# Performance work log

Measured on AMD Instinct MI355X. Metric: run time of the kernel, lower is better.

Reference implementation:

```python
import jax, jax.numpy as jnp
import numpy as np

NUM_NODES = 100000   # KG entity count (embedding table)
N_SUB = 20000        # subgraph nodes
E = 400000           # edges
R = 16               # num_rels
B = 8                # num_bases (block-diagonal decomposition)
H = 256              # h_dim (submat = H // B = 32)
PAIRS = 4096         # DTI drug-target pairs


def _rgcn_bdd_layer(x, src, dst, etype, norm, W, loop_w, bias):
    """DGL RelGraphConv with 'bdd' regularizer, self_loop=True, activation=None.

    message_e = blockdiag(W[etype_e]) @ x[src_e] * norm_e ; out_v = sum_e->v message_e
    By linearity we first segment-sum norm-scaled source features per (dst, rel)
    bucket, then apply the R relation block transforms once per node -- same math,
    no per-edge weight gather.
    """
    N, h = x.shape
    si = h // B  # block input size == block output size here
    contrib = x[src] * norm                      # [E, H]
    seg = dst * R + etype                        # bucket per (dst node, relation)
    agg = jax.ops.segment_sum(contrib, seg, num_segments=N * R)
    agg = agg.reshape(N, R, B, si)               # [N, R, B, si]
    msg = jnp.einsum('nrbi,rbio->nbo', agg, W).reshape(N, h)
    return msg + bias + x @ loop_w               # self-loop + bias (activation=None)


def setup_inputs() -> dict:
    key = jax.random.key(0)
    ks = jax.random.split(key, 20)
    si = H // B
    inp = {
        'drugs_index': jax.random.randint(ks[0], (PAIRS,), 0, N_SUB, dtype=jnp.int32),
        'targets_index': jax.random.randint(ks[1], (PAIRS,), 0, N_SUB, dtype=jnp.int32),
        'node_ids': jax.random.randint(ks[2], (N_SUB,), 0, NUM_NODES, dtype=jnp.int32),
        'src': jax.random.randint(ks[3], (E,), 0, N_SUB, dtype=jnp.int32),
        'dst': jax.random.randint(ks[4], (E,), 0, N_SUB, dtype=jnp.int32),
        'etype': jax.random.randint(ks[5], (E,), 0, R, dtype=jnp.int32),
        'norm': jax.random.uniform(ks[6], (E, 1), dtype=jnp.float32),
    }
    s_h = 1.0 / np.sqrt(H)
    s_blk = 1.0 / np.sqrt(si)
    inp['emb'] = jax.random.normal(ks[7], (NUM_NODES, H), jnp.float32)
    inp['w1'] = jax.random.normal(ks[8], (R, B, si, si), jnp.float32) * s_blk
    inp['loop_w1'] = jax.random.normal(ks[9], (H, H), jnp.float32) * s_h
    inp['b1'] = jnp.zeros((H,), jnp.float32)
    inp['w2'] = jax.random.normal(ks[10], (R, B, si, si), jnp.float32) * s_blk
    inp['loop_w2'] = jax.random.normal(ks[11], (H, H), jnp.float32) * s_h
    inp['b2'] = jnp.zeros((H,), jnp.float32)
    d = 2 * H
    inp['fc1_W'] = jax.random.normal(ks[12], (d, d), jnp.float32) / np.sqrt(d)
    inp['fc1_b'] = jnp.zeros((d,), jnp.float32)
    inp['fc2_W'] = jax.random.normal(ks[13], (d, 1), jnp.float32) / np.sqrt(d)
    inp['fc2_b'] = jnp.zeros((1,), jnp.float32)
    return inp


def reference(drugs_index, targets_index, node_ids, src, dst, etype, norm,
              emb, w1, loop_w1, b1, w2, loop_w2, b2,
              fc1_W, fc1_b, fc2_W, fc2_b):
    h = emb[node_ids]                                      # EmbeddingLayer
    h = _rgcn_bdd_layer(h, src, dst, etype, norm, w1, loop_w1, b1)
    h = _rgcn_bdd_layer(h, src, dst, etype, norm, w2, loop_w2, b2)
    x = jnp.concatenate([h[drugs_index], h[targets_index]], axis=1)  # [PAIRS, 2H]
    x = jax.nn.relu(x @ fc1_W + fc1_b)                     # dropout=0 -> identity
    return jax.nn.sigmoid(x @ fc2_W + fc2_b)               # [PAIRS, 1]
```

## Files before the change

### kernel.cpp

```cpp
#include <hip/hip_runtime.h>
#include <math.h>

typedef __attribute__((ext_vector_type(8))) short short8;
typedef __attribute__((ext_vector_type(4))) float f32x4;
typedef __attribute__((ext_vector_type(4))) _Float16 half4;
typedef __attribute__((ext_vector_type(8))) _Float16 half8;

#define N_SUBN   20000
#define E_EDGES  400000
#define R_REL    16
#define H_DIM    256
#define NBINS    (N_SUBN * R_REL)
#define SCAN_CHUNK 2048
#define NSCAN_BLOCKS ((NBINS + SCAN_CHUNK - 1) / SCAN_CHUNK)
#define NPAIRS   4096
#define TILE_N   32
#define NT_BLOCKS (N_SUBN / TILE_N)
#define D2       512
#define ECAP     1024

__device__ __forceinline__ ushort f2bf(float x) {
    uint u = __float_as_uint(x);
    u += 0x7fffu + ((u >> 16) & 1u);
    return (ushort)(u >> 16);
}
__device__ __forceinline__ float bf2f(ushort h) {
    return __uint_as_float(((uint)h) << 16);
}

__global__ void k_count(const int* __restrict__ dst, const int* __restrict__ ety,
                        int* __restrict__ cnt) {
    int e = blockIdx.x * 256 + threadIdx.x;
    if (e < E_EDGES) atomicAdd(&cnt[dst[e] * R_REL + ety[e]], 1);
}

__global__ void k_scan1(int* __restrict__ data, int* __restrict__ bs) {
    __shared__ int ts[256];
    int base = blockIdx.x * SCAN_CHUNK + threadIdx.x * 8;
    int v[8]; int s = 0;
#pragma unroll
    for (int j = 0; j < 8; j++) {
        int idx = base + j;
        v[j] = (idx < NBINS) ? data[idx] : 0;
        s += v[j];
    }
    ts[threadIdx.x] = s;
    __syncthreads();
    for (int off = 1; off < 256; off <<= 1) {
        int add = (threadIdx.x >= (unsigned)off) ? ts[threadIdx.x - off] : 0;
        __syncthreads();
        ts[threadIdx.x] += add;
        __syncthreads();
    }
    int excl = ts[threadIdx.x] - s;
    if (threadIdx.x == 255) bs[blockIdx.x] = ts[255];
    int run = excl;
#pragma unroll
    for (int j = 0; j < 8; j++) {
        int idx = base + j;
        if (idx < NBINS) data[idx] = run;
        run += v[j];
    }
}

__global__ void k_scan2(int* __restrict__ bs) {
    __shared__ int ls[NSCAN_BLOCKS];
    if (threadIdx.x < NSCAN_BLOCKS) ls[threadIdx.x] = bs[threadIdx.x];
    __syncthreads();
    if (threadIdx.x == 0) {
        int run = 0;
        for (int i = 0; i < NSCAN_BLOCKS; i++) { int t = ls[i]; ls[i] = run; run += t; }
    }
    __syncthreads();
    if (threadIdx.x < NSCAN_BLOCKS) bs[threadIdx.x] = ls[threadIdx.x];
}

__global__ void k_scan3(int* __restrict__ data, const int* __restrict__ bs) {
    int idx = blockIdx.x * 256 + threadIdx.x;
    if (idx < NBINS) data[idx] = data[idx] + bs[idx / SCAN_CHUNK];
}

__global__ void k_scatter(const int* __restrict__ src, const int* __restrict__ dst,
                          const int* __restrict__ ety, const float* __restrict__ nrm,
                          int* __restrict__ segend, uint* __restrict__ es) {
    int e = blockIdx.x * 256 + threadIdx.x;
    if (e >= E_EDGES) return;
    int bin = dst[e] * R_REL + ety[e];
    int pos = atomicAdd(&segend[bin], 1);
    float n = nrm[e];
    uint q = (uint)fminf(n * 131072.f + 0.5f, 131071.f);
    es[pos] = ((uint)src[e] << 17) | q;
}

__device__ __forceinline__ void prep_w_body(const float* __restrict__ w,
                                            ushort* __restrict__ wfrag, int t) {
    int lane = t & 63, f = t >> 6;
    int ot = f & 1, rb = f >> 1;
    int kbase = (lane >> 4) * 8, n = ot * 16 + (lane & 15);
    ushort hv[8], lv[8];
#pragma unroll
    for (int j = 0; j < 8; j++) {
        float x = w[(size_t)(rb * 32 + kbase + j) * 32 + n];
        ushort h = f2bf(x);
        ushort l = f2bf(x - bf2f(h));
        hv[j] = h; lv[j] = l;
    }
    *reinterpret_cast<short8*>(wfrag + ((size_t)(f * 2 + 0) * 64 + lane) * 8) =
        *reinterpret_cast<short8*>(hv);
    *reinterpret_cast<short8*>(wfrag + ((size_t)(f * 2 + 1) * 64 + lane) * 8) =
        *reinterpret_cast<short8*>(lv);
}

__device__ __forceinline__ void prep_lw_body(const float* __restrict__ lw,
                                             ushort* __restrict__ lwfrag, int t) {
    int lane = t & 63, g = t >> 6;
    int kt = g >> 4, ot = g & 15;
    int kbase = kt * 32 + (lane >> 4) * 8, n = ot * 16 + (lane & 15);
    ushort hv[8], lv[8];
#pragma unroll
    for (int j = 0; j < 8; j++) {
        float x = lw[(size_t)(kbase + j) * H_DIM + n];
        ushort h = f2bf(x);
        ushort l = f2bf(x - bf2f(h));
        hv[j] = h; lv[j] = l;
    }
    *reinterpret_cast<short8*>(lwfrag + ((size_t)(g * 2 + 0) * 64 + lane) * 8) =
        *reinterpret_cast<short8*>(hv);
    *reinterpret_cast<short8*>(lwfrag + ((size_t)(g * 2 + 1) * 64 + lane) * 8) =
        *reinterpret_cast<short8*>(lv);
}

__device__ __forceinline__ void prep_fc1_body(const float* __restrict__ w,
                                              ushort* __restrict__ wfrag, int t) {
    int lane = t & 63, g = t >> 6;
    int kt = g >> 5, ot = g & 31;
    int kbase = kt * 32 + (lane >> 4) * 8, n = ot * 16 + (lane & 15);
    ushort hv[8], lv[8];
#pragma unroll
    for (int j = 0; j < 8; j++) {
        float x = w[(size_t)(kbase + j) * D2 + n];
        ushort h = f2bf(x);
        ushort l = f2bf(x - bf2f(h));
        hv[j] = h; lv[j] = l;
    }
    *reinterpret_cast<short8*>(wfrag + ((size_t)(g * 2 + 0) * 64 + lane) * 8) =
        *reinterpret_cast<short8*>(hv);
    *reinterpret_cast<short8*>(wfrag + ((size_t)(g * 2 + 1) * 64 + lane) * 8) =
        *reinterpret_cast<short8*>(lv);
}

#define ZBLOCKS ((NBINS + 255) / 256)
#define GBLOCKS 5000
#define PREP_GRID (320 + ZBLOCKS + GBLOCKS)

__global__ void k_prep_all(const float* __restrict__ w1, const float* __restrict__ w2,
                           const float* __restrict__ lw1, const float* __restrict__ lw2,
                           const float* __restrict__ fc1W,
                           const float* __restrict__ emb, const int* __restrict__ nid,
                           ushort* __restrict__ wfrag1, ushort* __restrict__ wfrag2,
                           ushort* __restrict__ lwfrag1, ushort* __restrict__ lwfrag2,
                           ushort* __restrict__ fc1frag, int* __restrict__ segend,
                           _Float16* __restrict__ h0) {
    int b = blockIdx.x, tid = threadIdx.x;
    if (b < 64)        prep_w_body(w1, wfrag1, b * 256 + tid);
    else if (b < 128)  prep_w_body(w2, wfrag2, (b - 64) * 256 + tid);
    else if (b < 160)  prep_lw_body(lw1, lwfrag1, (b - 128) * 256 + tid);
    else if (b < 192)  prep_lw_body(lw2, lwfrag2, (b - 160) * 256 + tid);
    else if (b < 320)  prep_fc1_body(fc1W, fc1frag, (b - 192) * 256 + tid);
    else if (b < 320 + ZBLOCKS) {
        int i = (b - 320) * 256 + tid;
        if (i < NBINS) segend[i] = 0;
    } else {
        int t = (b - 320 - ZBLOCKS) * 256 + tid;
        int node = t >> 6, c = (t & 63) << 2;
        if (node < N_SUBN) {
            const float4 s = *reinterpret_cast<const float4*>(
                emb + (size_t)nid[node] * H_DIM + c);
            half4 d = {(_Float16)s.x, (_Float16)s.y, (_Float16)s.z, (_Float16)s.w};
            *reinterpret_cast<half4*>(h0 + (size_t)node * H_DIM + c) = d;
        }
    }
}

__global__ __launch_bounds__(512) void k_layer(
    const _Float16* __restrict__ hin, const uint* __restrict__ es,
    const int* __restrict__ segend,
    const ushort* __restrict__ wfrag, const ushort* __restrict__ lwfrag,
    const float* __restrict__ bias, _Float16* __restrict__ hout) {
    __shared__ __align__(16) ushort aggH[TILE_N * H_DIM];
    __shared__ __align__(16) ushort aggLo[TILE_N * H_DIM];
    __shared__ int lofs[TILE_N * R_REL + 1];
    __shared__ uint les[ECAP];
    char* cH = (char*)aggH;
    char* cL = (char*)aggLo;
    const int n0 = blockIdx.x * TILE_N;
    const int tid = threadIdx.x;
    const int lane = tid & 63, wv = tid >> 6;
    const int col = lane & 15, kg = lane >> 4;
    const short8* wf  = (const short8*)wfrag;
    const short8* lwf = (const short8*)lwfrag;
    const uint laneoff = (uint)(lane << 2);
    const int t0 = 4 * wv;

    {
        const int base = n0 * R_REL;
        for (int j = tid; j < TILE_N * R_REL + 1; j += 512) {
            int g = base + j - 1;
            lofs[j] = (g < 0) ? 0 : segend[g];
        }
    }
    __syncthreads();
    const int ebase = lofs[0];
    const int elim  = min(lofs[TILE_N * R_REL] - ebase, ECAP);
    for (int j = tid; j < elim; j += 512) les[j] = es[ebase + j];

    f32x4 acc[2][2];
#pragma unroll
    for (int mt = 0; mt < 2; ++mt)
#pragma unroll
        for (int ot = 0; ot < 2; ++ot) acc[mt][ot] = (f32x4){0.f, 0.f, 0.f, 0.f};

    for (int r = 0; r < R_REL; ++r) {
        __syncthreads();
        int e0 = lofs[(t0 + 0) * R_REL + r], d0 = lofs[(t0 + 0) * R_REL + r + 1];
        int e1 = lofs[(t0 + 1) * R_REL + r], d1 = lofs[(t0 + 1) * R_REL + r + 1];
        int e2 = lofs[(t0 + 2) * R_REL + r], d2 = lofs[(t0 + 2) * R_REL + r + 1];
        int e3 = lofs[(t0 + 3) * R_REL + r], d3 = lofs[(t0 + 3) * R_REL + r + 1];
        float4 a0 = make_float4(0.f, 0.f, 0.f, 0.f);
        float4 a1 = make_float4(0.f, 0.f, 0.f, 0.f);
        float4 a2 = make_float4(0.f, 0.f, 0.f, 0.f);
        float4 a3 = make_float4(0.f, 0.f, 0.f, 0.f);
        while ((e0 < d0) | (e1 < d1) | (e2 < d2) | (e3 < d3)) {
            bool g0 = e0 < d0, g1 = e1 < d1, g2 = e2 < d2, g3 = e3 < d3;
            uint p0 = 0, p1 = 0, p2 = 0, p3 = 0;
            if (g0) { int i = e0 - ebase; p0 = (i < ECAP) ? les[i] : es[e0]; ++e0; }
            if (g1) { int i = e1 - ebase; p1 = (i < ECAP) ? les[i] : es[e1]; ++e1; }
            if (g2) { int i = e2 - ebase; p2 = (i < ECAP) ? les[i] : es[e2]; ++e2; }
            if (g3) { int i = e3 - ebase; p3 = (i < ECAP) ? les[i] : es[e3]; ++e3; }
            if (g0) {
                const half4 x = *reinterpret_cast<const half4*>(
                    hin + (size_t)(p0 >> 17) * H_DIM + laneoff);
                float nm = (float)(p0 & 0x1FFFFu) * (1.f / 131072.f);
                a0.x = fmaf((float)x[0], nm, a0.x); a0.y = fmaf((float)x[1], nm, a0.y);
                a0.z = fmaf((float)x[2], nm, a0.z); a0.w = fmaf((float)x[3], nm, a0.w);
            }
            if (g1) {
                const half4 x = *reinterpret_cast<const half4*>(
                    hin + (size_t)(p1 >> 17) * H_DIM + laneoff);
                float nm = (float)(p1 & 0x1FFFFu) * (1.f / 131072.f);
                a1.x = fmaf((float)x[0], nm, a1.x); a1.y = fmaf((float)x[1], nm, a1.y);
                a1.z = fmaf((float)x[2], nm, a1.z); a1.w = fmaf((float)x[3], nm, a1.w);
            }
            if (g2) {
                const half4 x = *reinterpret_cast<const half4*>(
                    hin + (size_t)(p2 >> 17) * H_DIM + laneoff);
                float nm = (float)(p2 & 0x1FFFFu) * (1.f / 131072.f);
                a2.x = fmaf((float)x[0], nm, a2.x); a2.y = fmaf((float)x[1], nm, a2.y);
                a2.z = fmaf((float)x[2], nm, a2.z); a2.w = fmaf((float)x[3], nm, a2.w);
            }
            if (g3) {
                const half4 x = *reinterpret_cast<const half4*>(
                    hin + (size_t)(p3 >> 17) * H_DIM + laneoff);
                float nm = (float)(p3 & 0x1FFFFu) * (1.f / 131072.f);
                a3.x = fmaf((float)x[0], nm, a3.x); a3.y = fmaf((float)x[1], nm, a3.y);
                a3.z = fmaf((float)x[2], nm, a3.z); a3.w = fmaf((float)x[3], nm, a3.w);
            }
        }
#pragma unroll
        for (int i = 0; i < 4; ++i) {
            float4 av = (i == 0) ? a0 : (i == 1) ? a1 : (i == 2) ? a2 : a3;
            int t = t0 + i;
            ushort h0 = f2bf(av.x), h1 = f2bf(av.y), h2 = f2bf(av.z), h3 = f2bf(av.w);
            uint2 ph = make_uint2((uint)h0 | ((uint)h1 << 16), (uint)h2 | ((uint)h3 << 16));
            uint2 pl = make_uint2(
                (uint)f2bf(av.x - bf2f(h0)) | ((uint)f2bf(av.y - bf2f(h1)) << 16),
                (uint)f2bf(av.z - bf2f(h2)) | ((uint)f2bf(av.w - bf2f(h3)) << 16));
            uint byte = (uint)(t * 512) + ((((lane >> 1) ^ (t & 7)) << 4) | ((lane & 1) << 3));
            *(uint2*)(cH + byte) = ph;
            *(uint2*)(cL + byte) = pl;
        }
        __syncthreads();
#pragma unroll
        for (int ot = 0; ot < 2; ++ot) {
            int f = (r * 8 + wv) * 2 + ot;
            short8 Bh = wf[(f * 2 + 0) * 64 + lane];
            short8 Bl = wf[(f * 2 + 1) * 64 + lane];
#pragma unroll
            for (int mt = 0; mt < 2; ++mt) {
                int row = mt * 16 + col;
                uint ab = (uint)(row * 512) + ((uint)((wv * 4 + kg) ^ (row & 7)) << 4);
                short8 Ah = *(const short8*)(cH + ab);
                short8 Al = *(const short8*)(cL + ab);
                f32x4 a = acc[mt][ot];
                a = __builtin_amdgcn_mfma_f32_16x16x32_bf16(Ah, Bh, a, 0, 0, 0);
                a = __builtin_amdgcn_mfma_f32_16x16x32_bf16(Ah, Bl, a, 0, 0, 0);
                a = __builtin_amdgcn_mfma_f32_16x16x32_bf16(Al, Bh, a, 0, 0, 0);
                acc[mt][ot] = a;
            }
        }
    }

    __syncthreads();
#pragma unroll
    for (int i = 0; i < 4; ++i) {
        int t = t0 + i;
        const half4 xh = *reinterpret_cast<const half4*>(
            hin + (size_t)(n0 + t) * H_DIM + laneoff);
        float4 xv = make_float4((float)xh[0], (float)xh[1], (float)xh[2], (float)xh[3]);
        ushort h0 = f2bf(xv.x), h1 = f2bf(xv.y), h2 = f2bf(xv.z), h3 = f2bf(xv.w);
        uint2 ph = make_uint2((uint)h0 | ((uint)h1 << 16), (uint)h2 | ((uint)h3 << 16));
        uint2 pl = make_uint2(
            (uint)f2bf(xv.x - bf2f(h0)) | ((uint)f2bf(xv.y - bf2f(h1)) << 16),
            (uint)f2bf(xv.z - bf2f(h2)) | ((uint)f2bf(xv.w - bf2f(h3)) << 16));
        uint byte = (uint)(t * 512) + ((((lane >> 1) ^ (t & 7)) << 4) | ((lane & 1) << 3));
        *(uint2*)(cH + byte) = ph;
        *(uint2*)(cL + byte) = pl;
    }
    __syncthreads();
#pragma unroll
    for (int kt = 0; kt < 8; ++kt) {
#pragma unroll
        for (int ot = 0; ot < 2; ++ot) {
            int g = kt * 16 + 2 * wv + ot;
            short8 Bh = lwf[(g * 2 + 0) * 64 + lane];
            short8 Bl = lwf[(g * 2 + 1) * 64 + lane];
#pragma unroll
            for (int mt = 0; mt < 2; ++mt) {
                int row = mt * 16 + col;
                uint ab = (uint)(row * 512) + ((uint)((kt * 4 + kg) ^ (row & 7)) << 4);
                short8 Ah = *(const short8*)(cH + ab);
                short8 Al = *(const short8*)(cL + ab);
                f32x4 a = acc[mt][ot];
                a = __builtin_amdgcn_mfma_f32_16x16x32_bf16(Ah, Bh, a, 0, 0, 0);
                a = __builtin_amdgcn_mfma_f32_16x16x32_bf16(Ah, Bl, a, 0, 0, 0);
                a = __builtin_amdgcn_mfma_f32_16x16x32_bf16(Al, Bh, a, 0, 0, 0);
                acc[mt][ot] = a;
            }
        }
    }

#pragma unroll
    for (int mt = 0; mt < 2; ++mt) {
        int nbase = n0 + mt * 16 + kg * 4;
#pragma unroll
        for (int ot = 0; ot < 2; ++ot) {
            int o = 32 * wv + ot * 16 + col;
            float bo = bias[o];
#pragma unroll
            for (int rg = 0; rg < 4; ++rg)
                hout[(size_t)(nbase + rg) * H_DIM + o] = (_Float16)(acc[mt][ot][rg] + bo);
        }
    }
}

__global__ __launch_bounds__(512) void k_mlp(
    const _Float16* __restrict__ h, const int* __restrict__ drugs,
    const int* __restrict__ targets,
    const ushort* __restrict__ fc1frag, const float* __restrict__ b1f,
    const float* __restrict__ W2, const float* __restrict__ b2f,
    float* __restrict__ outp) {
    __shared__ __align__(16) ushort xH[16 * D2];
    __shared__ __align__(16) ushort xL[16 * D2];
    __shared__ float red[16][8];
    char* cH = (char*)xH;
    char* cL = (char*)xL;
    const int tid = threadIdx.x;
    const int lane = tid & 63, wv = tid >> 6;
    const int col = lane & 15, kg = lane >> 4;
    const int p0 = blockIdx.x * 16;
    const short8* wf = (const short8*)fc1frag;

    {
        int p = tid >> 5;
        int cc = (tid & 31) * 16;
        int di = drugs[p0 + p], ti = targets[p0 + p];
        const _Float16* srcp = (cc < H_DIM) ? (h + (size_t)di * H_DIM + cc)
                                            : (h + (size_t)ti * H_DIM + (cc - H_DIM));
#pragma unroll
        for (int j = 0; j < 2; ++j) {
            half8 v = *reinterpret_cast<const half8*>(srcp + j * 8);
            float f[8];
#pragma unroll
            for (int q = 0; q < 8; ++q) f[q] = (float)v[q];
            short8 hv, lv;
#pragma unroll
            for (int q = 0; q < 8; ++q) {
                ushort hh = f2bf(f[q]);
                hv[q] = (short)hh;
                lv[q] = (short)f2bf(f[q] - bf2f(hh));
            }
            uint chunk = (uint)((tid & 31) * 2 + j);
            uint byte = (uint)p * 1024 + ((chunk ^ (uint)(p & 7)) << 4);
            *(short8*)(cH + byte) = hv;
            *(short8*)(cL + byte) = lv;
        }
    }
    __syncthreads();

    f32x4 acc[4];
#pragma unroll
    for (int oi = 0; oi < 4; ++oi) acc[oi] = (f32x4){0.f, 0.f, 0.f, 0.f};

    for (int kt = 0; kt < 16; ++kt) {
        uint ab = (uint)col * 1024 + ((uint)((kt * 4 + kg) ^ (col & 7)) << 4);
        short8 Ah = *(const short8*)(cH + ab);
        short8 Al = *(const short8*)(cL + ab);
#pragma unroll
        for (int oi = 0; oi < 4; ++oi) {
            int g = kt * 32 + wv * 4 + oi;
            short8 Bh = wf[(g * 2 + 0) * 64 + lane];
            short8 Bl = wf[(g * 2 + 1) * 64 + lane];
            f32x4 a = acc[oi];
            a = __builtin_amdgcn_mfma_f32_16x16x32_bf16(Ah, Bh, a, 0, 0, 0);
            a = __builtin_amdgcn_mfma_f32_16x16x32_bf16(Ah, Bl, a, 0, 0, 0);
            a = __builtin_amdgcn_mfma_f32_16x16x32_bf16(Al, Bh, a, 0, 0, 0);
            a = __builtin_amdgcn_mfma_f32_16x16x32_bf16(Al, Bl, a, 0, 0, 0);
            acc[oi] = a;
        }
    }

    float val[4] = {0.f, 0.f, 0.f, 0.f};
#pragma unroll
    for (int oi = 0; oi < 4; ++oi) {
        int o = 64 * wv + oi * 16 + col;
        float b1o = b1f[o], w2o = W2[o];
#pragma unroll
        for (int rg = 0; rg < 4; ++rg) {
            float y = acc[oi][rg] + b1o;
            y = y > 0.f ? y : 0.f;
            val[rg] = fmaf(y, w2o, val[rg]);
        }
    }
#pragma unroll
    for (int rg = 0; rg < 4; ++rg) {
        float v = val[rg];
        v += __shfl_xor(v, 1, 64);
        v += __shfl_xor(v, 2, 64);
        v += __shfl_xor(v, 4, 64);
        v += __shfl_xor(v, 8, 64);
        val[rg] = v;
    }
    if (col == 0) {
#pragma unroll
        for (int rg = 0; rg < 4; ++rg) red[kg * 4 + rg][wv] = val[rg];
    }
    __syncthreads();
    if (tid < 16) {
        float s = 0.f;
#pragma unroll
        for (int w = 0; w < 8; w++) s += red[tid][w];
        s += b2f[0];
        outp[p0 + tid] = 1.f / (1.f + __expf(-s));
    }
}

extern "C" void kernel_launch(void* const* d_in, const int* in_sizes, int n_in,
                              void* d_out, int out_size, void* d_ws, size_t ws_size,
                              hipStream_t stream) {
    (void)in_sizes; (void)n_in; (void)out_size; (void)ws_size;
    const int*   drugs   = (const int*)d_in[0];
    const int*   targets = (const int*)d_in[1];
    const int*   nid     = (const int*)d_in[2];
    const int*   src     = (const int*)d_in[3];
    const int*   dst     = (const int*)d_in[4];
    const int*   ety     = (const int*)d_in[5];
    const float* nrm     = (const float*)d_in[6];
    const float* emb     = (const float*)d_in[7];
    const float* w1      = (const float*)d_in[8];
    const float* lw1     = (const float*)d_in[9];
    const float* b1      = (const float*)d_in[10];
    const float* w2      = (const float*)d_in[11];
    const float* lw2     = (const float*)d_in[12];
    const float* b2      = (const float*)d_in[13];
    const float* fc1W    = (const float*)d_in[14];
    const float* fc1b    = (const float*)d_in[15];
    const float* fc2W    = (const float*)d_in[16];
    const float* fc2b    = (const float*)d_in[17];
    float* outp = (float*)d_out;

    char* ws = (char*)d_ws;
    ushort*   wfrag1  = (ushort*)  (ws);
    ushort*   wfrag2  = (ushort*)  (ws + 524288);
    ushort*   lwfrag1 = (ushort*)  (ws + 1048576);
    ushort*   lwfrag2 = (ushort*)  (ws + 1310720);
    ushort*   fc1frag = (ushort*)  (ws + 1572864);
    _Float16* hA      = (_Float16*)(ws + 2621440);
    _Float16* hB      = (_Float16*)(ws + 23101440);
    int*      segend  = (int*)     (ws + 43581440);
    int*      bs      = (int*)     (ws + 44861440);
    uint*     es      = (uint*)    (ws + 44862464);

    k_prep_all<<<PREP_GRID, 256, 0, stream>>>(w1, w2, lw1, lw2, fc1W, emb, nid,
                                              wfrag1, wfrag2, lwfrag1, lwfrag2,
                                              fc1frag, segend, hA);
    k_count  <<<(E_EDGES + 255) / 256, 256, 0, stream>>>(dst, ety, segend);
    k_scan1  <<<NSCAN_BLOCKS, 256, 0, stream>>>(segend, bs);
    k_scan2  <<<1, 256, 0, stream>>>(bs);
    k_scan3  <<<(NBINS + 255) / 256, 256, 0, stream>>>(segend, bs);
    k_scatter<<<(E_EDGES + 255) / 256, 256, 0, stream>>>(src, dst, ety, nrm, segend, es);
    k_layer  <<<NT_BLOCKS, 512, 0, stream>>>(hA, es, segend, wfrag1, lwfrag1, b1, hB);
    k_layer  <<<NT_BLOCKS, 512, 0, stream>>>(hB, es, segend, wfrag2, lwfrag2, b2, hA);
    k_mlp    <<<NPAIRS / 16, 512, 0, stream>>>(hA, drugs, targets, fc1frag, fc1b, fc2W, fc2b, outp);
}
```

Measured before the change: 265.5 us.

## Split layer relations across two blocks per tile and combine partial outputs

Each node tile is now handled by two blocks. One block aggregates relations 0-7, the other handles relations 8-15 plus the self-loop and bias. Each writes an fp16 partial result, and a new elementwise kernel sums the two partials into the layer output. This doubles the grid from 625 to 1250 blocks so more CUs are busy. The cost is an extra kernel launch per layer, the extra partial-buffer traffic, and one more fp16 rounding step in the combine.

```diff
diff --git a/kernel.cpp b/kernel.cpp
--- a/kernel.cpp
+++ b/kernel.cpp
@@ -186,14 +186,17 @@
     const _Float16* __restrict__ hin, const uint* __restrict__ es,
     const int* __restrict__ segend,
     const ushort* __restrict__ wfrag, const ushort* __restrict__ lwfrag,
-    const float* __restrict__ bias, _Float16* __restrict__ hout) {
+    const float* __restrict__ bias,
+    _Float16* __restrict__ pA, _Float16* __restrict__ pB) {
     __shared__ __align__(16) ushort aggH[TILE_N * H_DIM];
     __shared__ __align__(16) ushort aggLo[TILE_N * H_DIM];
     __shared__ int lofs[TILE_N * R_REL + 1];
     __shared__ uint les[ECAP];
     char* cH = (char*)aggH;
     char* cL = (char*)aggLo;
-    const int n0 = blockIdx.x * TILE_N;
+    const int bid = blockIdx.x;
+    const int half_ = bid & 1;
+    const int n0 = (bid >> 1) * TILE_N;
     const int tid = threadIdx.x;
     const int lane = tid & 63, wv = tid >> 6;
     const int col = lane & 15, kg = lane >> 4;
@@ -220,7 +223,9 @@
 #pragma unroll
         for (int ot = 0; ot < 2; ++ot) acc[mt][ot] = (f32x4){0.f, 0.f, 0.f, 0.f};
 
-    for (int r = 0; r < R_REL; ++r) {
+    const int rbase = half_ * 8;
+    for (int rr = 0; rr < 8; ++rr) {
+        const int r = rbase + rr;
         __syncthreads();
         int e0 = lofs[(t0 + 0) * R_REL + r], d0 = lofs[(t0 + 0) * R_REL + r + 1];
         int e1 = lofs[(t0 + 1) * R_REL + r], d1 = lofs[(t0 + 1) * R_REL + r + 1];
@@ -300,57 +305,71 @@
         }
     }
 
-    __syncthreads();
-#pragma unroll
-    for (int i = 0; i < 4; ++i) {
-        int t = t0 + i;
-        const half4 xh = *reinterpret_cast<const half4*>(
-            hin + (size_t)(n0 + t) * H_DIM + laneoff);
-        float4 xv = make_float4((float)xh[0], (float)xh[1], (float)xh[2], (float)xh[3]);
-        ushort h0 = f2bf(xv.x), h1 = f2bf(xv.y), h2 = f2bf(xv.z), h3 = f2bf(xv.w);
-        uint2 ph = make_uint2((uint)h0 | ((uint)h1 << 16), (uint)h2 | ((uint)h3 << 16));
-        uint2 pl = make_uint2(
-            (uint)f2bf(xv.x - bf2f(h0)) | ((uint)f2bf(xv.y - bf2f(h1)) << 16),
-            (uint)f2bf(xv.z - bf2f(h2)) | ((uint)f2bf(xv.w - bf2f(h3)) << 16));
-        uint byte = (uint)(t * 512) + ((((lane >> 1) ^ (t & 7)) << 4) | ((lane & 1) << 3));
-        *(uint2*)(cH + byte) = ph;
-        *(uint2*)(cL + byte) = pl;
-    }
-    __syncthreads();
-#pragma unroll
-    for (int kt = 0; kt < 8; ++kt) {
-#pragma unroll
-        for (int ot = 0; ot < 2; ++ot) {
-            int g = kt * 16 + 2 * wv + ot;
-            short8 Bh = lwf[(g * 2 + 0) * 64 + lane];
-            short8 Bl = lwf[(g * 2 + 1) * 64 + lane];
-#pragma unroll
-            for (int mt = 0; mt < 2; ++mt) {
-                int row = mt * 16 + col;
-                uint ab = (uint)(row * 512) + ((uint)((kt * 4 + kg) ^ (row & 7)) << 4);
-                short8 Ah = *(const short8*)(cH + ab);
-                short8 Al = *(const short8*)(cL + ab);
-                f32x4 a = acc[mt][ot];
-                a = __builtin_amdgcn_mfma_f32_16x16x32_bf16(Ah, Bh, a, 0, 0, 0);
-                a = __builtin_amdgcn_mfma_f32_16x16x32_bf16(Ah, Bl, a, 0, 0, 0);
-                a = __builtin_amdgcn_mfma_f32_16x16x32_bf16(Al, Bh, a, 0, 0, 0);
-                acc[mt][ot] = a;
-            }
-        }
-    }
-
+    if (half_) {
+        __syncthreads();
+#pragma unroll
+        for (int i = 0; i < 4; ++i) {
+            int t = t0 + i;
+            const half4 xh = *reinterpret_cast<const half4*>(
+                hin + (size_t)(n0 + t) * H_DIM + laneoff);
+            float4 xv = make_float4((float)xh[0], (float)xh[1], (float)xh[2], (float)xh[3]);
+            ushort h0 = f2bf(xv.x), h1 = f2bf(xv.y), h2 = f2bf(xv.z), h3 = f2bf(xv.w);
+            uint2 ph = make_uint2((uint)h0 | ((uint)h1 << 16), (uint)h2 | ((uint)h3 << 16));
+            uint2 pl = make_uint2(
+                (uint)f2bf(xv.x - bf2f(h0)) | ((uint)f2bf(xv.y - bf2f(h1)) << 16),
+                (uint)f2bf(xv.z - bf2f(h2)) | ((uint)f2bf(xv.w - bf2f(h3)) << 16));
+            uint byte = (uint)(t * 512) + ((((lane >> 1) ^ (t & 7)) << 4) | ((lane & 1) << 3));
+            *(uint2*)(cH + byte) = ph;
+            *(uint2*)(cL + byte) = pl;
+        }
+        __syncthreads();
+#pragma unroll
+        for (int kt = 0; kt < 8; ++kt) {
+#pragma unroll
+            for (int ot = 0; ot < 2; ++ot) {
+                int g = kt * 16 + 2 * wv + ot;
+                short8 Bh = lwf[(g * 2 + 0) * 64 + lane];
+                short8 Bl = lwf[(g * 2 + 1) * 64 + lane];
+#pragma unroll
+                for (int mt = 0; mt < 2; ++mt) {
+                    int row = mt * 16 + col;
+                    uint ab = (uint)(row * 512) + ((uint)((kt * 4 + kg) ^ (row & 7)) << 4);
+                    short8 Ah = *(const short8*)(cH + ab);
+                    short8 Al = *(const short8*)(cL + ab);
+                    f32x4 a = acc[mt][ot];
+                    a = __builtin_amdgcn_mfma_f32_16x16x32_bf16(Ah, Bh, a, 0, 0, 0);
+                    a = __builtin_amdgcn_mfma_f32_16x16x32_bf16(Ah, Bl, a, 0, 0, 0);
+                    a = __builtin_amdgcn_mfma_f32_16x16x32_bf16(Al, Bh, a, 0, 0, 0);
+                    acc[mt][ot] = a;
+                }
+            }
+        }
+    }
+
+    _Float16* out = half_ ? pB : pA;
 #pragma unroll
     for (int mt = 0; mt < 2; ++mt) {
         int nbase = n0 + mt * 16 + kg * 4;
 #pragma unroll
         for (int ot = 0; ot < 2; ++ot) {
             int o = 32 * wv + ot * 16 + col;
-            float bo = bias[o];
+            float bo = half_ ? bias[o] : 0.f;
 #pragma unroll
             for (int rg = 0; rg < 4; ++rg)
-                hout[(size_t)(nbase + rg) * H_DIM + o] = (_Float16)(acc[mt][ot][rg] + bo);
-        }
-    }
+                out[(size_t)(nbase + rg) * H_DIM + o] = (_Float16)(acc[mt][ot][rg] + bo);
+        }
+    }
+}
+
+__global__ void k_comb(const _Float16* __restrict__ pA, const _Float16* __restrict__ pB,
+                       _Float16* __restrict__ out) {
+    size_t i = ((size_t)blockIdx.x * 256 + threadIdx.x) * 8;
+    half8 a = *reinterpret_cast<const half8*>(pA + i);
+    half8 b = *reinterpret_cast<const half8*>(pB + i);
+    half8 c;
+#pragma unroll
+    for (int q = 0; q < 8; ++q) c[q] = (_Float16)((float)a[q] + (float)b[q]);
+    *reinterpret_cast<half8*>(out + i) = c;
 }
 
 __global__ __launch_bounds__(512) void k_mlp(
@@ -485,7 +504,9 @@
     ushort*   lwfrag2 = (ushort*)  (ws + 1310720);
     ushort*   fc1frag = (ushort*)  (ws + 1572864);
     _Float16* hA      = (_Float16*)(ws + 2621440);
-    _Float16* hB      = (_Float16*)(ws + 23101440);
+    _Float16* hB      = (_Float16*)(ws + 12861440);
+    _Float16* pA      = (_Float16*)(ws + 23101440);
+    _Float16* pB      = (_Float16*)(ws + 33341440);
     int*      segend  = (int*)     (ws + 43581440);
     int*      bs      = (int*)     (ws + 44861440);
     uint*     es      = (uint*)    (ws + 44862464);
@@ -498,7 +519,9 @@
     k_scan2  <<<1, 256, 0, stream>>>(bs);
     k_scan3  <<<(NBINS + 255) / 256, 256, 0, stream>>>(segend, bs);
     k_scatter<<<(E_EDGES + 255) / 256, 256, 0, stream>>>(src, dst, ety, nrm, segend, es);
-    k_layer  <<<NT_BLOCKS, 512, 0, stream>>>(hA, es, segend, wfrag1, lwfrag1, b1, hB);
-    k_layer  <<<NT_BLOCKS, 512, 0, stream>>>(hB, es, segend, wfrag2, lwfrag2, b2, hA);
+    k_layer  <<<2 * NT_BLOCKS, 512, 0, stream>>>(hA, es, segend, wfrag1, lwfrag1, b1, pA, pB);
+    k_comb   <<<2500, 256, 0, stream>>>(pA, pB, hB);
+    k_layer  <<<2 * NT_BLOCKS, 512, 0, stream>>>(hB, es, segend, wfrag2, lwfrag2, b2, pA, pB);
+    k_comb   <<<2500, 256, 0, stream>>>(pA, pB, hA);
     k_mlp    <<<NPAIRS / 16, 512, 0, stream>>>(hA, drugs, targets, fc1frag, fc1b, fc2W, fc2b, outp);
 }
```

Result: slower. 282.0 us (+6.2%).
